# Optimization experiments

Hardware: AMD Instinct MI355X
Metric: run time of the kernel (lower is better)

Reference implementation:

```python
import jax, jax.numpy as jnp
import numpy as np

N_NODES = 50000

def setup_inputs() -> dict:
    key = jax.random.key(0)
    k1, k2, k3, k4, k5, k6 = jax.random.split(key, 6)
    T, D, N, E = 10000, 128, N_NODES, 800000
    impact = jax.random.normal(k1, (T, D), dtype=jnp.float32)
    W = jax.random.normal(k2, (D, D), dtype=jnp.float32)
    M = jax.random.normal(k3, (D, D), dtype=jnp.float32)
    node_ids = jax.random.randint(k4, (N,), 0, T, dtype=jnp.int64)
    neighbor_ids = jax.random.randint(k5, (E,), 0, T, dtype=jnp.int64)
    neighbor_segments = jnp.sort(jax.random.randint(k6, (E,), 0, N, dtype=jnp.int64))
    return {"impact": impact, "W": W, "M": M, "node_ids": node_ids,
            "neighbor_ids": neighbor_ids, "neighbor_segments": neighbor_segments}

def reference(impact, W, M, node_ids, neighbor_ids, neighbor_segments):
    # Per node i (type k_i): s_i = relu(W @ h[k_i] + sum_{j in N(i)} M @ h[type_j])
    # result = softmax(sum_i s_i) over the D feature axis.
    self_feats = impact[node_ids]                          # (N, D) gather
    neigh_feats = impact[neighbor_ids]                     # (E, D) gather
    neigh_sum = jax.ops.segment_sum(neigh_feats, neighbor_segments,
                                    num_segments=N_NODES)  # (N, D) scatter-add
    pre = self_feats @ W.T + neigh_sum @ M.T               # (N, D)
    result = jnp.sum(jax.nn.relu(pre), axis=0)             # (D,)
    return jax.nn.softmax(result, axis=0)
```

## Files before the change

### kernel.cpp

```cpp
#include <hip/hip_runtime.h>

#define DDIM 128
#define ACC_BLOCKS 2048
#define NHALF (ACC_BLOCKS * 4 * 2)
#define RED_BLOCKS 64

typedef unsigned int uint;
typedef unsigned short ushort;
typedef __attribute__((ext_vector_type(8))) short bf16x8;
typedef __attribute__((ext_vector_type(4))) float f32x4;

static __device__ __forceinline__ ushort f2bf(float x) {
    uint u = __float_as_uint(x);
    u += 0x7fffu + ((u >> 16) & 1u);
    return (ushort)(u >> 16);
}
static __device__ __forceinline__ float bflo(uint u) { return __uint_as_float(u << 16); }
static __device__ __forceinline__ float bfhi(uint u) { return __uint_as_float(u & 0xffff0000u); }

__global__ __launch_bounds__(256) void prep(
    const int* __restrict__ segs,
    const int* __restrict__ node_ids,
    const int* __restrict__ neighbor_ids,
    int* __restrict__ rowptr,
    int* __restrict__ items,
    int* __restrict__ done,
    float* __restrict__ zrow,
    int N, int E, int whoff, int mhoff, int zpad)
{
    const int x = blockIdx.x * blockDim.x + threadIdx.x;
    if (x == 0) *done = 0;
    if (x < 64) zrow[x] = 0.f;
    if (x >= E) return;

    const int sc = segs[x];
    const int sp = (x == 0) ? -1 : segs[x - 1];
    const int sn = (x + 1 < E) ? segs[x + 1] : N;

    items[x + sc + 1] = (mhoff + neighbor_ids[x] * 256) | ((sn != sc) ? (int)0x80000000 : 0);

    for (int i = sp + 1; i <= sc; ++i) {
        rowptr[i] = x;
        items[x + i] = (whoff + node_ids[i] * 256) | ((i < sc) ? (int)0x80000000 : 0);
    }
    if (x == E - 1) {
        for (int i = sc + 1; i <= N; ++i) {
            rowptr[i] = E;
            if (i < N) items[E + i] = (whoff + node_ids[i] * 256) | (int)0x80000000;
        }
#pragma unroll
        for (int q = 0; q < 16; ++q) items[N + E + q] = zpad;
    }
}

static __device__ __forceinline__ bf16x8 load_frag8(const float* base) {
    const float4 p = *reinterpret_cast<const float4*>(base);
    const float4 q = *reinterpret_cast<const float4*>(base + 4);
    bf16x8 f;
    f[0] = (short)f2bf(p.x); f[1] = (short)f2bf(p.y);
    f[2] = (short)f2bf(p.z); f[3] = (short)f2bf(p.w);
    f[4] = (short)f2bf(q.x); f[5] = (short)f2bf(q.y);
    f[6] = (short)f2bf(q.z); f[7] = (short)f2bf(q.w);
    return f;
}

__global__ __launch_bounds__(256) void precompute_mfma(
    const float* __restrict__ impact,
    const float* __restrict__ W,
    const float* __restrict__ Mm,
    ushort* __restrict__ WhB,
    ushort* __restrict__ MhB,
    const int* __restrict__ rowptr,
    int* __restrict__ wstart,
    int T, int N, int K)
{
    const int gid = blockIdx.x * 256 + threadIdx.x;
    if (gid <= NHALF) {
        const int t = (int)(((long long)gid * K) / NHALF);
        int lo = 0, hi = N;
        while (lo < hi) {
            const int mid = (lo + hi) >> 1;
            if (rowptr[mid] + mid < t) lo = mid + 1; else hi = mid;
        }
        wstart[gid] = rowptr[lo] + lo;
    }

    const int lane = threadIdx.x & 63;
    const int wv   = threadIdx.x >> 6;
    const int t0   = blockIdx.x * 32;
    const int r16  = lane & 15;
    const int kg   = lane >> 4;

    bf16x8 A[2][4];
#pragma unroll
    for (int rt = 0; rt < 2; ++rt) {
        int t = t0 + rt * 16 + r16;
        if (t >= T) t = T - 1;
        const float* abase = impact + (size_t)t * DDIM + kg * 8;
#pragma unroll
        for (int k0i = 0; k0i < 4; ++k0i)
            A[rt][k0i] = load_frag8(abase + k0i * 32);
    }

#pragma unroll
    for (int dti = 0; dti < 2; ++dti) {
        const int d0 = (wv * 2 + dti) * 16;
#pragma unroll
        for (int m = 0; m < 2; ++m) {
            const float* mat = (m == 0) ? W : Mm;
            ushort* out = (m == 0) ? WhB : MhB;
            const float* bbase = mat + (size_t)(d0 + r16) * DDIM + kg * 8;
            f32x4 acc0 = {0.f, 0.f, 0.f, 0.f};
            f32x4 acc1 = {0.f, 0.f, 0.f, 0.f};
#pragma unroll
            for (int k0i = 0; k0i < 4; ++k0i) {
                const bf16x8 b = load_frag8(bbase + k0i * 32);
                acc0 = __builtin_amdgcn_mfma_f32_16x16x32_bf16(A[0][k0i], b, acc0, 0, 0, 0);
                acc1 = __builtin_amdgcn_mfma_f32_16x16x32_bf16(A[1][k0i], b, acc1, 0, 0, 0);
            }
            const int dcol = d0 + r16;
#pragma unroll
            for (int r = 0; r < 4; ++r) {
                const int tr0 = t0 + kg * 4 + r;
                const int tr1 = tr0 + 16;
                if (tr0 < T) out[(size_t)tr0 * DDIM + dcol] = f2bf(acc0[r]);
                if (tr1 < T) out[(size_t)tr1 * DDIM + dcol] = f2bf(acc1[r]);
            }
        }
    }
}

__global__ __launch_bounds__(256, 8) void accumulate_items(
    const char* __restrict__ tab,
    const int* __restrict__ items,
    const int* __restrict__ wstart,
    float* __restrict__ partials,
    int zpad)
{
    const int tid  = threadIdx.x;
    const int lane = tid & 63;
    const int wv   = __builtin_amdgcn_readfirstlane(tid >> 6);
    const int w    = blockIdx.x * 4 + wv;

    int kA        = __builtin_amdgcn_readfirstlane(wstart[2 * w]);
    const int kAe = __builtin_amdgcn_readfirstlane(wstart[2 * w + 1]);
    int kB        = kAe;
    const int kBe = __builtin_amdgcn_readfirstlane(wstart[2 * w + 2]);

    const bool isB  = lane >= 32;
    const uint vbase = (uint)(lane & 31) * 8u;

    float c0 = 0.f, c1 = 0.f, c2 = 0.f, c3 = 0.f;
    float a0 = 0.f, a1 = 0.f, a2 = 0.f, a3 = 0.f;

    while (kA < kAe || kB < kBe) {
        int wA[8], wB[8];
        if (kA + 8 <= kAe && kB + 8 <= kBe) {
#pragma unroll
            for (int j = 0; j < 8; ++j) { wA[j] = items[kA + j]; wB[j] = items[kB + j]; }
        } else {
#pragma unroll
            for (int j = 0; j < 8; ++j) {
                wA[j] = (kA + j < kAe) ? items[kA + j] : zpad;
                wB[j] = (kB + j < kBe) ? items[kB + j] : zpad;
            }
        }
        uint2 v[8];
#pragma unroll
        for (int j = 0; j < 8; ++j) {
            const uint off = ((uint)(isB ? wB[j] : wA[j]) & 0x7fffffffu) + vbase;
            v[j] = *reinterpret_cast<const uint2*>(tab + off);
        }
#pragma unroll
        for (int j = 0; j < 8; ++j) {
            c0 += bflo(v[j].x); c1 += bfhi(v[j].x);
            c2 += bflo(v[j].y); c3 += bfhi(v[j].y);
            const bool fA = wA[j] < 0;
            const bool fB = wB[j] < 0;
            if (__builtin_amdgcn_ballot_w64(1) && (fA || fB)) {
                const bool myf = isB ? fB : fA;
                a0 += myf ? fmaxf(c0, 0.f) : 0.f;
                a1 += myf ? fmaxf(c1, 0.f) : 0.f;
                a2 += myf ? fmaxf(c2, 0.f) : 0.f;
                a3 += myf ? fmaxf(c3, 0.f) : 0.f;
                c0 = myf ? 0.f : c0;  c1 = myf ? 0.f : c1;
                c2 = myf ? 0.f : c2;  c3 = myf ? 0.f : c3;
            }
        }
        kA = min(kA + 8, kAe);
        kB = min(kB + 8, kBe);
    }
    a0 += fmaxf(c0, 0.f); a1 += fmaxf(c1, 0.f);
    a2 += fmaxf(c2, 0.f); a3 += fmaxf(c3, 0.f);

    __shared__ float red[8][DDIM];
    *reinterpret_cast<float4*>(&red[wv * 2 + (isB ? 1 : 0)][(lane & 31) * 4]) =
        make_float4(a0, a1, a2, a3);
    __syncthreads();
    if (tid < DDIM) {
        float s = 0.f;
#pragma unroll
        for (int g = 0; g < 8; ++g) s += red[g][tid];
        partials[(size_t)blockIdx.x * DDIM + tid] = s;
    }
}

__global__ __launch_bounds__(256) void reduce_softmax(
    const float* __restrict__ partials, float* __restrict__ out2,
    float* __restrict__ out, int* __restrict__ done, int nb)
{
    const int tid = threadIdx.x;
    const int d = tid & (DDIM - 1);
    const int h = tid >> 7;
    {
        const int rows = nb / RED_BLOCKS;
        const int r0 = blockIdx.x * rows;
        float s = 0.f;
        for (int r = r0 + h; r < r0 + rows; r += 2)
            s += partials[(size_t)r * DDIM + d];
        __shared__ float red[2][DDIM];
        red[h][d] = s;
        __syncthreads();
        if (tid < DDIM)
            out2[(size_t)blockIdx.x * DDIM + tid] = red[0][tid] + red[1][tid];
    }
    __threadfence();
    __shared__ int isLast;
    if (tid == 0) {
        const int v = atomicAdd(done, 1);
        isLast = (v == RED_BLOCKS - 1) ? 1 : 0;
    }
    __syncthreads();
    if (!isLast) return;
    __threadfence();

    float s = 0.f;
    for (int b = h; b < RED_BLOCKS; b += 2)
        s += out2[(size_t)b * DDIM + d];
    __shared__ float r2[2][DDIM];
    r2[h][d] = s;
    __syncthreads();

    __shared__ float vec[DDIM];
    __shared__ float tmp[DDIM];
    if (tid < DDIM) { const float v = r2[0][tid] + r2[1][tid]; vec[tid] = v; tmp[tid] = v; }
    __syncthreads();
    for (int o = 64; o > 0; o >>= 1) {
        if (tid < o) tmp[tid] = fmaxf(tmp[tid], tmp[tid + o]);
        __syncthreads();
    }
    const float mx = tmp[0];
    __syncthreads();
    float ev = 0.f;
    if (tid < DDIM) { ev = expf(vec[tid] - mx); tmp[tid] = ev; }
    __syncthreads();
    for (int o = 64; o > 0; o >>= 1) {
        if (tid < o) tmp[tid] += tmp[tid + o];
        __syncthreads();
    }
    if (tid < DDIM) out[tid] = ev / tmp[0];
}

extern "C" void kernel_launch(void* const* d_in, const int* in_sizes, int n_in,
                              void* d_out, int out_size, void* d_ws, size_t ws_size,
                              hipStream_t stream) {
    const float* impact        = (const float*)d_in[0];
    const float* W             = (const float*)d_in[1];
    const float* Mm            = (const float*)d_in[2];
    const int*   node_ids      = (const int*)d_in[3];
    const int*   neighbor_ids  = (const int*)d_in[4];
    const int*   neighbor_segs = (const int*)d_in[5];

    const int T = in_sizes[0] / DDIM;
    const int N = in_sizes[3];
    const int E = in_sizes[4];
    const int K = N + E;

    char* ws = (char*)d_ws;
    size_t off = 0;
    const int whoff = (int)off;
    ushort* WhB = (ushort*)(ws + off);  off += (size_t)T * DDIM * sizeof(ushort);
    const int mhoff = (int)off;
    ushort* MhB = (ushort*)(ws + off);  off += (size_t)T * DDIM * sizeof(ushort);
    const int zoff = (int)off;
    float* zrow = (float*)(ws + off);   off += 64 * sizeof(float);
    float* partials = (float*)(ws + off); off += (size_t)ACC_BLOCKS * DDIM * sizeof(float);
    float* part2    = (float*)(ws + off); off += (size_t)RED_BLOCKS * DDIM * sizeof(float);
    int*   rowptr   = (int*)(ws + off);   off += (size_t)(N + 1) * sizeof(int);
    int*   done     = (int*)(ws + off);   off += 256;
    off = (off + 255) & ~(size_t)255;
    int*   items    = (int*)(ws + off);   off += (size_t)(K + 16) * sizeof(int);
    int*   wstart   = (int*)(ws + off);   off += (size_t)(NHALF + 1) * sizeof(int);
    float* outf     = (float*)d_out;

    prep<<<(E + 255) / 256, 256, 0, stream>>>(
        neighbor_segs, node_ids, neighbor_ids, rowptr, items, done, zrow,
        N, E, whoff, mhoff, zoff);
    precompute_mfma<<<(T + 31) / 32, 256, 0, stream>>>(
        impact, W, Mm, WhB, MhB, rowptr, wstart, T, N, K);
    accumulate_items<<<ACC_BLOCKS, 256, 0, stream>>>(ws, items, wstart, partials, zoff);
    reduce_softmax<<<RED_BLOCKS, 256, 0, stream>>>(partials, part2, outf, done, ACC_BLOCKS);
}
```

Measured before the change: 71.01 us.

## Store projected tables in fp16, accumulate with packed half2, double-buffer gathers

The projected W·h and M·h tables are now stored as fp16 instead of bf16. Segment sums are accumulated with packed __hadd2 instructions, which halves the per-element add work. The accumulate loop is software-pipelined with two register buffers, so the next batch of item loads and gathers is issued before the current batch is reduced, and the bounds-check branch is replaced by unconditional loads with select. Padding grows to 32 items to cover the over-read. The risk is reduced precision and possible overflow from summing in fp16 over long segments, plus higher register pressure.

```diff
diff --git a/kernel.cpp b/kernel.cpp
--- a/kernel.cpp
+++ b/kernel.cpp
@@ -1,8 +1,10 @@
 #include <hip/hip_runtime.h>
+#include <hip/hip_fp16.h>
 
 #define DDIM 128
 #define ACC_BLOCKS 2048
-#define NHALF (ACC_BLOCKS * 4 * 2)
+#define NWAVES (ACC_BLOCKS * 4)
+#define NHALF (NWAVES * 2)
 #define RED_BLOCKS 64
 
 typedef unsigned int uint;
@@ -15,8 +17,6 @@
     u += 0x7fffu + ((u >> 16) & 1u);
     return (ushort)(u >> 16);
 }
-static __device__ __forceinline__ float bflo(uint u) { return __uint_as_float(u << 16); }
-static __device__ __forceinline__ float bfhi(uint u) { return __uint_as_float(u & 0xffff0000u); }
 
 __global__ __launch_bounds__(256) void prep(
     const int* __restrict__ segs,
@@ -25,12 +25,12 @@
     int* __restrict__ rowptr,
     int* __restrict__ items,
     int* __restrict__ done,
-    float* __restrict__ zrow,
+    uint* __restrict__ zrow,
     int N, int E, int whoff, int mhoff, int zpad)
 {
     const int x = blockIdx.x * blockDim.x + threadIdx.x;
     if (x == 0) *done = 0;
-    if (x < 64) zrow[x] = 0.f;
+    if (x < 64) zrow[x] = 0u;
     if (x >= E) return;
 
     const int sc = segs[x];
@@ -49,7 +49,7 @@
             if (i < N) items[E + i] = (whoff + node_ids[i] * 256) | (int)0x80000000;
         }
 #pragma unroll
-        for (int q = 0; q < 16; ++q) items[N + E + q] = zpad;
+        for (int q = 0; q < 32; ++q) items[N + E + q] = zpad;
     }
 }
 
@@ -68,8 +68,8 @@
     const float* __restrict__ impact,
     const float* __restrict__ W,
     const float* __restrict__ Mm,
-    ushort* __restrict__ WhB,
-    ushort* __restrict__ MhB,
+    __half* __restrict__ WhH,
+    __half* __restrict__ MhH,
     const int* __restrict__ rowptr,
     int* __restrict__ wstart,
     int T, int N, int K)
@@ -108,7 +108,7 @@
 #pragma unroll
         for (int m = 0; m < 2; ++m) {
             const float* mat = (m == 0) ? W : Mm;
-            ushort* out = (m == 0) ? WhB : MhB;
+            __half* out = (m == 0) ? WhH : MhH;
             const float* bbase = mat + (size_t)(d0 + r16) * DDIM + kg * 8;
             f32x4 acc0 = {0.f, 0.f, 0.f, 0.f};
             f32x4 acc1 = {0.f, 0.f, 0.f, 0.f};
@@ -123,14 +123,14 @@
             for (int r = 0; r < 4; ++r) {
                 const int tr0 = t0 + kg * 4 + r;
                 const int tr1 = tr0 + 16;
-                if (tr0 < T) out[(size_t)tr0 * DDIM + dcol] = f2bf(acc0[r]);
-                if (tr1 < T) out[(size_t)tr1 * DDIM + dcol] = f2bf(acc1[r]);
+                if (tr0 < T) out[(size_t)tr0 * DDIM + dcol] = __float2half(acc0[r]);
+                if (tr1 < T) out[(size_t)tr1 * DDIM + dcol] = __float2half(acc1[r]);
             }
         }
     }
 }
 
-__global__ __launch_bounds__(256, 8) void accumulate_items(
+__global__ __launch_bounds__(256, 8) void accumulate_pairs(
     const char* __restrict__ tab,
     const int* __restrict__ items,
     const int* __restrict__ wstart,
@@ -147,54 +147,78 @@
     int kB        = kAe;
     const int kBe = __builtin_amdgcn_readfirstlane(wstart[2 * w + 2]);
 
-    const bool isB  = lane >= 32;
-    const uint vbase = (uint)(lane & 31) * 8u;
-
-    float c0 = 0.f, c1 = 0.f, c2 = 0.f, c3 = 0.f;
+    const bool inB = lane >= 32;
+    const uint vb  = (uint)(lane & 31) * 8u;
+
+    const __half2 z2 = __floats2half2_rn(0.f, 0.f);
+    __half2 c0 = z2, c1 = z2;
     float a0 = 0.f, a1 = 0.f, a2 = 0.f, a3 = 0.f;
 
-    while (kA < kAe || kB < kBe) {
-        int wA[8], wB[8];
-        if (kA + 8 <= kAe && kB + 8 <= kBe) {
-#pragma unroll
-            for (int j = 0; j < 8; ++j) { wA[j] = items[kA + j]; wB[j] = items[kB + j]; }
-        } else {
-#pragma unroll
-            for (int j = 0; j < 8; ++j) {
-                wA[j] = (kA + j < kAe) ? items[kA + j] : zpad;
-                wB[j] = (kB + j < kBe) ? items[kB + j] : zpad;
-            }
+#define LOADI8(WA, WB) { \
+    _Pragma("unroll") \
+    for (int j = 0; j < 8; ++j) { \
+        const int ta_ = items[kA + j]; \
+        const int tb_ = items[kB + j]; \
+        WA[j] = (kA + j < kAe) ? ta_ : zpad; \
+        WB[j] = (kB + j < kBe) ? tb_ : zpad; \
+    } \
+    kA = min(kA + 8, kAe); \
+    kB = min(kB + 8, kBe); }
+
+#define GATHER8(V, WA, WB) { \
+    _Pragma("unroll") \
+    for (int j = 0; j < 8; ++j) { \
+        const int sa_ = WA[j] & 0x7fffffff; \
+        const int sb_ = WB[j] & 0x7fffffff; \
+        const uint off_ = (uint)(inB ? sb_ : sa_) + vb; \
+        V[j] = *reinterpret_cast<const uint2*>(tab + off_); \
+    } }
+
+#define ACC8(V, WA, WB) { \
+    _Pragma("unroll") \
+    for (int j = 0; j < 8; ++j) { \
+        c0 = __hadd2(c0, *reinterpret_cast<const __half2*>(&V[j].x)); \
+        c1 = __hadd2(c1, *reinterpret_cast<const __half2*>(&V[j].y)); \
+        const bool fA_ = WA[j] < 0; \
+        const bool fB_ = WB[j] < 0; \
+        if (fA_ || fB_) { \
+            const bool myf_ = inB ? fB_ : fA_; \
+            if (myf_) { \
+                const float2 f0_ = __half22float2(c0); \
+                const float2 f1_ = __half22float2(c1); \
+                a0 += fmaxf(f0_.x, 0.f); a1 += fmaxf(f0_.y, 0.f); \
+                a2 += fmaxf(f1_.x, 0.f); a3 += fmaxf(f1_.y, 0.f); \
+                c0 = z2; c1 = z2; \
+            } \
+        } \
+    } }
+
+    if (kA < kAe || kB < kBe) {
+        int wa0[8], wb0[8], wa1[8], wb1[8];
+        uint2 v0[8], v1[8];
+        LOADI8(wa0, wb0);
+        GATHER8(v0, wa0, wb0);
+        for (;;) {
+            const bool more1 = (kA < kAe) || (kB < kBe);
+            if (more1) { LOADI8(wa1, wb1); GATHER8(v1, wa1, wb1); }
+            ACC8(v0, wa0, wb0);
+            if (!more1) break;
+            const bool more2 = (kA < kAe) || (kB < kBe);
+            if (more2) { LOADI8(wa0, wb0); GATHER8(v0, wa0, wb0); }
+            ACC8(v1, wa1, wb1);
+            if (!more2) break;
         }
-        uint2 v[8];
-#pragma unroll
-        for (int j = 0; j < 8; ++j) {
-            const uint off = ((uint)(isB ? wB[j] : wA[j]) & 0x7fffffffu) + vbase;
-            v[j] = *reinterpret_cast<const uint2*>(tab + off);
-        }
-#pragma unroll
-        for (int j = 0; j < 8; ++j) {
-            c0 += bflo(v[j].x); c1 += bfhi(v[j].x);
-            c2 += bflo(v[j].y); c3 += bfhi(v[j].y);
-            const bool fA = wA[j] < 0;
-            const bool fB = wB[j] < 0;
-            if (__builtin_amdgcn_ballot_w64(1) && (fA || fB)) {
-                const bool myf = isB ? fB : fA;
-                a0 += myf ? fmaxf(c0, 0.f) : 0.f;
-                a1 += myf ? fmaxf(c1, 0.f) : 0.f;
-                a2 += myf ? fmaxf(c2, 0.f) : 0.f;
-                a3 += myf ? fmaxf(c3, 0.f) : 0.f;
-                c0 = myf ? 0.f : c0;  c1 = myf ? 0.f : c1;
-                c2 = myf ? 0.f : c2;  c3 = myf ? 0.f : c3;
-            }
-        }
-        kA = min(kA + 8, kAe);
-        kB = min(kB + 8, kBe);
-    }
-    a0 += fmaxf(c0, 0.f); a1 += fmaxf(c1, 0.f);
-    a2 += fmaxf(c2, 0.f); a3 += fmaxf(c3, 0.f);
+    }
+
+    {
+        const float2 f0 = __half22float2(c0);
+        const float2 f1 = __half22float2(c1);
+        a0 += fmaxf(f0.x, 0.f); a1 += fmaxf(f0.y, 0.f);
+        a2 += fmaxf(f1.x, 0.f); a3 += fmaxf(f1.y, 0.f);
+    }
 
     __shared__ float red[8][DDIM];
-    *reinterpret_cast<float4*>(&red[wv * 2 + (isB ? 1 : 0)][(lane & 31) * 4]) =
+    *reinterpret_cast<float4*>(&red[wv * 2 + (inB ? 1 : 0)][(lane & 31) * 4]) =
         make_float4(a0, a1, a2, a3);
     __syncthreads();
     if (tid < DDIM) {
@@ -279,17 +303,17 @@
     char* ws = (char*)d_ws;
     size_t off = 0;
     const int whoff = (int)off;
-    ushort* WhB = (ushort*)(ws + off);  off += (size_t)T * DDIM * sizeof(ushort);
+    __half* WhH = (__half*)(ws + off);  off += (size_t)T * DDIM * sizeof(__half);
     const int mhoff = (int)off;
-    ushort* MhB = (ushort*)(ws + off);  off += (size_t)T * DDIM * sizeof(ushort);
+    __half* MhH = (__half*)(ws + off);  off += (size_t)T * DDIM * sizeof(__half);
     const int zoff = (int)off;
-    float* zrow = (float*)(ws + off);   off += 64 * sizeof(float);
+    uint* zrow = (uint*)(ws + off);     off += 64 * sizeof(uint);
     float* partials = (float*)(ws + off); off += (size_t)ACC_BLOCKS * DDIM * sizeof(float);
     float* part2    = (float*)(ws + off); off += (size_t)RED_BLOCKS * DDIM * sizeof(float);
     int*   rowptr   = (int*)(ws + off);   off += (size_t)(N + 1) * sizeof(int);
     int*   done     = (int*)(ws + off);   off += 256;
     off = (off + 255) & ~(size_t)255;
-    int*   items    = (int*)(ws + off);   off += (size_t)(K + 16) * sizeof(int);
+    int*   items    = (int*)(ws + off);   off += (size_t)(K + 32) * sizeof(int);
     int*   wstart   = (int*)(ws + off);   off += (size_t)(NHALF + 1) * sizeof(int);
     float* outf     = (float*)d_out;
 
@@ -297,7 +321,7 @@
         neighbor_segs, node_ids, neighbor_ids, rowptr, items, done, zrow,
         N, E, whoff, mhoff, zoff);
     precompute_mfma<<<(T + 31) / 32, 256, 0, stream>>>(
-        impact, W, Mm, WhB, MhB, rowptr, wstart, T, N, K);
-    accumulate_items<<<ACC_BLOCKS, 256, 0, stream>>>(ws, items, wstart, partials, zoff);
+        impact, W, Mm, WhH, MhH, rowptr, wstart, T, N, K);
+    accumulate_pairs<<<ACC_BLOCKS, 256, 0, stream>>>(ws, items, wstart, partials, zoff);
     reduce_softmax<<<RED_BLOCKS, 256, 0, stream>>>(partials, part2, outf, done, ACC_BLOCKS);
 }
```

After: 68.86 us. 3.0% less time.
